# Performance work log

Hardware: AMD Instinct MI355X
Metric: run time of the kernel (lower is better)

## Reference

```python
import jax, jax.numpy as jnp
import numpy as np

N = 16384
C = 4        # in_channels
K = 16       # neighbors
H = 64       # mlp width


def setup_inputs() -> dict:
    key = jax.random.key(0)
    k0, k1, k2, k3, k4 = jax.random.split(key, 5)
    x = jax.random.normal(k0, (N, C), dtype=jnp.float32)
    # nn.Linear(2C, 64) and nn.Linear(64, 64): weight [out, in], bias [out]
    W1 = jax.random.normal(k1, (H, 2 * C), dtype=jnp.float32) * (1.0 / np.sqrt(2 * C))
    b1 = jax.random.normal(k2, (H,), dtype=jnp.float32) * 0.01
    W2 = jax.random.normal(k3, (H, H), dtype=jnp.float32) * (1.0 / np.sqrt(H))
    b2 = jax.random.normal(k4, (H,), dtype=jnp.float32) * 0.01
    return {"x": x, "W1": W1, "b1": b1, "W2": W2, "b2": b2}


def reference(x, W1, b1, W2, b2):
    # x: [N, C] single point cloud (torch code unsqueezes batch dim 0)
    xs = jax.lax.stop_gradient(x)  # knn indices computed under no_grad
    # pairwise = -||xi - xj||^2 = 2*xi.xj - ||xi||^2 - ||xj||^2
    xx = jnp.sum(xs * xs, axis=1)                      # [N]
    pairwise = 2.0 * (xs @ xs.T) - xx[:, None] - xx[None, :]  # [N, N]
    _, idx = jax.lax.top_k(pairwise, K)                # [N, K] (self included, dist 0 is max)
    neigh = x[idx]                                     # [N, K, C] gather
    center = jnp.broadcast_to(x[:, None, :], (x.shape[0], K, C))
    edge = jnp.concatenate([neigh - center, center], axis=-1)  # [N, K, 2C]
    h = jax.nn.relu(jnp.einsum('nkc,hc->nkh', edge, W1) + b1)
    h = jax.nn.relu(jnp.einsum('nkh,gh->nkg', h, W2) + b2)     # [N, K, H]
    out = jnp.mean(h, axis=1)                          # [N, H]
    return out[None]                                   # [1, N, H] matches torch output
```

## Files before the change

### kernel.cpp

```cpp
#include <hip/hip_runtime.h>
#include <math.h>

#define N_PTS 16384
#define K_NBR 16
#define H_DIM 64
#define CAP   78
#define NBLK  (N_PTS / 16)
#define PBLK  (NBLK / 4)

typedef unsigned long long u64;
typedef unsigned short u16;
typedef float v2f   __attribute__((ext_vector_type(2)));
typedef float f32x4 __attribute__((ext_vector_type(4)));
typedef short bf16x8 __attribute__((ext_vector_type(8)));

__device__ __forceinline__ u64 mkkey(unsigned vbits, unsigned idx) {
    unsigned of = vbits ^ (unsigned)(((int)vbits >> 31) | 0x80000000);
    return ((u64)of << 32) | (unsigned)(~idx);
}
__device__ __forceinline__ unsigned keyidx(u64 k) { return ~(unsigned)k; }

__device__ __forceinline__ float readlane_f(float v, int l) {
    return __uint_as_float(__builtin_amdgcn_readlane(__float_as_uint(v), l));
}

__device__ __forceinline__ unsigned ofsbits(float f) {
    unsigned b = __float_as_uint(f);
    return b ^ ((unsigned)((int)b >> 31) | 0x80000000u);
}
__device__ __forceinline__ float inv_ofs(unsigned u) {
    return __uint_as_float(u ^ (~(unsigned)((int)u >> 31) | 0x80000000u));
}

__device__ __forceinline__ u16 f2bf(float f) {
    unsigned u = __float_as_uint(f);
    return (u16)((u + 0x7FFFu + ((u >> 16) & 1u)) >> 16);
}
__device__ __forceinline__ float bf2f(u16 b) {
    return __uint_as_float(((unsigned)b) << 16);
}

__device__ __forceinline__ float wave_sort_f32(float v, int lane) {
#pragma unroll
    for (int k = 2; k <= 64; k <<= 1) {
#pragma unroll
        for (int j = k >> 1; j > 0; j >>= 1) {
            float o = __shfl_xor(v, j, 64);
            bool keep_min = (((lane & k) == 0) == ((lane & j) == 0));
            v = keep_min ? fminf(v, o) : fmaxf(v, o);
        }
    }
    return v;
}
__device__ __forceinline__ u64 wave_sort_u64(u64 v, int lane) {
#pragma unroll
    for (int k = 2; k <= 64; k <<= 1) {
#pragma unroll
        for (int j = k >> 1; j > 0; j >>= 1) {
            u64 o = __shfl_xor((unsigned long long)v, j, 64);
            bool keep_min = (((lane & k) == 0) == ((lane & j) == 0));
            u64 mn = (v < o) ? v : o;
            u64 mx = (v < o) ? o : v;
            v = keep_min ? mn : mx;
        }
    }
    return v;
}

struct CompRes { int nc; float tau; };
__device__ __attribute__((noinline)) CompRes wave_compact(uint2* buf, int cnt,
                                                          int lane) {
    float lm = -INFINITY;
    for (int s = lane; s < cnt; s += 64)
        lm = fmaxf(lm, __uint_as_float(buf[s].x));
    const float tv = readlane_f(wave_sort_f32(lm, lane), 48);
    int nc = 0;
    for (int s0 = 0; s0 < cnt; s0 += 64) {
        const int s = s0 + lane;
        uint2 e = make_uint2(0u, 0u);
        bool keep = false;
        if (s < cnt) { e = buf[s]; keep = (__uint_as_float(e.x) >= tv); }
        const u64 km = __ballot(keep);
        if (keep) {
            int pfx = (int)__popcll(km & ((1ull << lane) - 1));
            buf[nc + pfx] = e;
        }
        nc += (int)__popcll(km);
    }
    CompRes r; r.nc = nc; r.tau = tv;
    return r;
}

__global__ __launch_bounds__(256) void prep_kernel(const float4* __restrict__ x4,
                                                   u16* __restrict__ bf) {
    const int i = blockIdx.x * 256 + threadIdx.x;
    const float4 v = x4[i];
    float xx;
    {
#pragma clang fp contract(off)
        float s0 = v.x * v.x, s1 = v.y * v.y, s2 = v.z * v.z, s3 = v.w * v.w;
        xx = ((s0 + s1) + s2) + s3;
    }
    float c[4] = {v.x, v.y, v.z, v.w};
    u16 H[4], M[4], L[4];
#pragma unroll
    for (int q = 0; q < 4; ++q) {
        float f = c[q];
        u16 h = f2bf(f);            float fh = bf2f(h);
        u16 m = f2bf(f - fh);       float fm = bf2f(m);
        u16 l = f2bf(f - fh - fm);
        H[q] = h; M[q] = m; L[q] = l;
    }
    const float nx = -xx;
    u16 X0 = f2bf(nx);              float x0f = bf2f(X0);
    u16 X1 = f2bf(nx - x0f);        float x1f = bf2f(X1);
    u16 X2 = f2bf(nx - x0f - x1f);
    u16 o[32];
#pragma unroll
    for (int q = 0; q < 4; ++q) {
        o[q]      = H[q];
        o[4 + q]  = M[q];
        o[8 + q]  = H[q];
        o[12 + q] = L[q];
        o[16 + q] = H[q];
        o[20 + q] = M[q];
    }
    o[24] = X0; o[25] = X1; o[26] = X2;
    o[27] = 0; o[28] = 0; o[29] = 0; o[30] = 0; o[31] = 0;
    uint4* dst = (uint4*)(bf + (size_t)i * 32);
#pragma unroll
    for (int q2 = 0; q2 < 4; ++q2) {
        uint4 w;
        w.x = (unsigned)o[q2 * 8 + 0] | ((unsigned)o[q2 * 8 + 1] << 16);
        w.y = (unsigned)o[q2 * 8 + 2] | ((unsigned)o[q2 * 8 + 3] << 16);
        w.z = (unsigned)o[q2 * 8 + 4] | ((unsigned)o[q2 * 8 + 5] << 16);
        w.w = (unsigned)o[q2 * 8 + 6] | ((unsigned)o[q2 * 8 + 7] << 16);
        dst[q2] = w;
    }
}

__global__ __launch_bounds__(256, 4) void knn_kernel(
        const float4* __restrict__ x4,
        const u16* __restrict__ bfrag,
        int* __restrict__ knn) {
    __shared__ __align__(16) uint2 buf[4][16][CAP];
    __shared__ unsigned tau_sh[16];
    const int lane = threadIdx.x & 63;
    const int wave = threadIdx.x >> 6;
    const int q    = lane & 15;
    const int g    = lane >> 4;
    const int rowbase = blockIdx.x * 16;
    const int pblk = wave * PBLK;

    const float4 xi = x4[rowbase + q];
    u16 Ha[4], Ma[4], La[4];
    {
        float yy[4] = {2.f * xi.x, 2.f * xi.y, 2.f * xi.z, 2.f * xi.w};
#pragma unroll
        for (int c = 0; c < 4; ++c) {
            u16 h = f2bf(yy[c]);             float fh = bf2f(h);
            u16 m = f2bf(yy[c] - fh);        float fm = bf2f(m);
            u16 l = f2bf(yy[c] - fh - fm);
            Ha[c] = h; Ma[c] = m; La[c] = l;
        }
    }
    bf16x8 qfrag;
    {
        const u16 ONEB = 0x3F80;
#pragma unroll
        for (int c = 0; c < 4; ++c) {
            u16 lo, hi;
            if (g == 0)      { lo = Ha[c]; hi = Ha[c]; }
            else if (g == 1) { lo = Ma[c]; hi = Ha[c]; }
            else if (g == 2) { lo = La[c]; hi = Ma[c]; }
            else             { lo = (c < 3) ? ONEB : 0; hi = 0; }
            qfrag[c]     = (short)lo;
            qfrag[c + 4] = (short)hi;
        }
    }
    const f32x4 zacc = {0.f, 0.f, 0.f, 0.f};
    const bf16x8* bp = (const bf16x8*)bfrag + (size_t)pblk * 64 + (q * 4 + g);

    f32x4 mx = {-INFINITY, -INFINITY, -INFINITY, -INFINITY};
    {
        bf16x8 A0[4], A1[4];
#pragma unroll
        for (int i = 0; i < 4; ++i) A0[i] = bp[(2 * i) * 64];
#pragma unroll
        for (int i = 0; i < 4; ++i) A1[i] = bp[(8 + 2 * i) * 64];
        const bf16x8* pa = bp + 16 * 64;

#define PROCA(BUF) do {                                                      \
    _Pragma("unroll")                                                        \
    for (int i = 0; i < 4; ++i) {                                            \
        const f32x4 aa = __builtin_amdgcn_mfma_f32_16x16x32_bf16(            \
            BUF[i], qfrag, zacc, 0, 0, 0);                                   \
        mx[0] = fmaxf(mx[0], aa[0]); mx[1] = fmaxf(mx[1], aa[1]);            \
        mx[2] = fmaxf(mx[2], aa[2]); mx[3] = fmaxf(mx[3], aa[3]);            \
    }                                                                        \
} while (0)

        for (int it = 0; it < 15; ++it) {
            PROCA(A0);
#pragma unroll
            for (int i = 0; i < 4; ++i) A0[i] = pa[(2 * i) * 64];
            PROCA(A1);
#pragma unroll
            for (int i = 0; i < 4; ++i) A1[i] = pa[(8 + 2 * i) * 64];
            pa += 16 * 64;
        }
        PROCA(A0);
        PROCA(A1);
#undef PROCA
    }

    {
        float* am = (float*)&buf[0][0][0];
        const int base = wave * 256 + q * 16 + g * 4;
        am[base + 0] = mx[0]; am[base + 1] = mx[1];
        am[base + 2] = mx[2]; am[base + 3] = mx[3];
        __syncthreads();
#pragma unroll
        for (int rr = 0; rr < 4; ++rr) {
            const int r = wave * 4 + rr;
            float v = am[(lane >> 4) * 256 + r * 16 + (lane & 15)];
            v = wave_sort_f32(v, lane);
            if (lane == 48) tau_sh[r] = ofsbits(v);
        }
        __syncthreads();
    }
    float tau = inv_ofs(tau_sh[q]);

    unsigned cq = 0;
    uint2* bq = &buf[wave][q][0];
    const unsigned gid4 = (unsigned)(g * 4);

#define INSERT4(AV, CB) do {                                                 \
    for (;;) {                                                               \
        const bool k0 = (AV)[0] >= tau, k1 = (AV)[1] >= tau;                 \
        const bool k2 = (AV)[2] >= tau, k3 = (AV)[3] >= tau;                 \
        const int cnt = (int)k0 + (int)k1 + (int)k2 + (int)k3;               \
        const int sa = __shfl_xor(cnt, 16, 64);                              \
        const int sb = __shfl_xor(cnt, 32, 64);                              \
        const int sc = __shfl_xor(sa, 32, 64);                               \
        const int tot = cnt + sa + sb + sc;                                  \
        const int pf  = ((g & 1) ? sa : 0) + ((g & 2) ? (sb + sc) : 0);      \
        const u64 ovm = __ballot(cq + (unsigned)tot > CAP);                  \
        if (__builtin_expect(ovm == 0, 1)) {                                 \
            unsigned slot = cq + (unsigned)pf;                               \
            if (k0) bq[slot++] = make_uint2(__float_as_uint((AV)[0]), (CB)); \
            if (k1) bq[slot++] = make_uint2(__float_as_uint((AV)[1]), (CB)+1);\
            if (k2) bq[slot++] = make_uint2(__float_as_uint((AV)[2]), (CB)+2);\
            if (k3) bq[slot++] = make_uint2(__float_as_uint((AV)[3]), (CB)+3);\
            cq += (unsigned)tot;                                             \
            break;                                                           \
        }                                                                    \
        u64 ov = ovm & 0xFFFFull;                                            \
        while (ov) {                                                         \
            const int r = (int)__builtin_ctzll(ov); ov &= ov - 1;            \
            const unsigned cr =                                              \
                (unsigned)__builtin_amdgcn_readlane((int)cq, r);             \
            CompRes res = wave_compact(&buf[wave][r][0], (int)cr, lane);     \
            if (q == r) { cq = (unsigned)res.nc;                             \
                          tau = fmaxf(tau, res.tau); }                       \
        }                                                                    \
    }                                                                        \
} while (0)

#define PROC4(BUF, TB) do {                                                  \
    f32x4 A4_[4];                                                            \
    _Pragma("unroll")                                                        \
    for (int i = 0; i < 4; ++i)                                              \
        A4_[i] = __builtin_amdgcn_mfma_f32_16x16x32_bf16(BUF[i], qfrag,      \
                                                         zacc, 0, 0, 0);     \
    _Pragma("unroll")                                                        \
    for (int i = 0; i < 4; ++i) {                                            \
        const f32x4 av = A4_[i];                                             \
        const float m4 = fmaxf(fmaxf(av[0], av[1]), fmaxf(av[2], av[3]));    \
        if (__ballot(m4 >= tau))                                             \
            INSERT4(av, (unsigned)(((TB) + i) * 16) + gid4);                 \
    }                                                                        \
} while (0)

    {
        bf16x8 B0[4], B1[4];
#pragma unroll
        for (int i = 0; i < 4; ++i) B0[i] = bp[i * 64];
#pragma unroll
        for (int i = 0; i < 4; ++i) B1[i] = bp[(4 + i) * 64];
        const bf16x8* pA = bp + 8 * 64;
        const bf16x8* pB = bp + 12 * 64;

        int t = 0;
        for (; t < PBLK - 8; t += 8) {
            PROC4(B0, pblk + t);
#pragma unroll
            for (int i = 0; i < 4; ++i) B0[i] = pA[i * 64];
            pA += 8 * 64;
            PROC4(B1, pblk + t + 4);
#pragma unroll
            for (int i = 0; i < 4; ++i) B1[i] = pB[i * 64];
            pB += 8 * 64;
        }
        PROC4(B0, pblk + t);
        PROC4(B1, pblk + t + 4);
    }
#undef PROC4
#undef INSERT4

#pragma unroll 1
    for (int r = 0; r < 16; ++r) {
        int c = __builtin_amdgcn_readlane((int)cq, r);
        uint2* br = &buf[wave][r][0];
        if (c > 64) { CompRes res = wave_compact(br, c, lane); c = res.nc; }
        if (c <= 16) {
            if (lane < 16) {
                u64 key = 0;
                if (lane < c) { const uint2 e = br[lane]; key = mkkey(e.x, e.y); }
                *(u64*)&buf[wave][r][lane] = key;
            }
        } else {
            u64 key = 0;
            if (lane < c) { const uint2 e = br[lane]; key = mkkey(e.x, e.y); }
            key = wave_sort_u64(key, lane);
            if (lane >= 48)
                *(u64*)&buf[wave][r][lane - 48] = key;
        }
    }

    __syncthreads();
#pragma unroll
    for (int rr = 0; rr < 4; ++rr) {
        const int r2 = wave * 4 + rr;
        u64 key = *(const u64*)&buf[lane >> 4][r2][lane & 15];
        key = wave_sort_u64(key, lane);
        if (lane >= 48)
            knn[(rowbase + r2) * K_NBR + (lane - 48)] = (int)keyidx(key);
    }
}

__global__ __launch_bounds__(256, 2) void mlp_kernel(
        const float4* __restrict__ x4,
        const int* __restrict__ knn,
        const float4* __restrict__ W2f4,
        const float* __restrict__ W1,
        const float* __restrict__ b1,
        const float* __restrict__ b2,
        float* __restrict__ out) {
    __shared__ __align__(16) float4 w2s[16][64];
    __shared__ __align__(16) float  h1s[4][32][68];
    __shared__ __align__(16) float4 xjs[4][32];
    const int lane = threadIdx.x & 63;
    const int wave = threadIdx.x >> 6;
    const int kq   = lane >> 4;
    const int gp   = lane & 15;
    const int p0   = (blockIdx.x * 4 + wave) * 2;

    for (int q = threadIdx.x; q < 1024; q += 256)
        w2s[q & 15][q >> 4] = W2f4[q];
    __syncthreads();

    float w1r[8];
#pragma unroll
    for (int c = 0; c < 8; ++c) w1r[c] = W1[lane * 8 + c];
    const float b1r = b1[lane];
    float b2r[4];
#pragma unroll
    for (int gq = 0; gq < 4; ++gq) b2r[gq] = b2[gq * 16 + gp];

    if (lane < 32) {
        const int pp = lane >> 4;
        const int nb = knn[(p0 + pp) * K_NBR + (lane & 15)];
        xjs[wave][lane] = x4[nb];
    }

#pragma unroll
    for (int pp = 0; pp < 2; ++pp) {
        const float4 xi = x4[p0 + pp];
        float hb = b1r;
        hb = fmaf(w1r[4] - w1r[0], xi.x, hb);
        hb = fmaf(w1r[5] - w1r[1], xi.y, hb);
        hb = fmaf(w1r[6] - w1r[2], xi.z, hb);
        hb = fmaf(w1r[7] - w1r[3], xi.w, hb);
#pragma unroll
        for (int k = 0; k < K_NBR; ++k) {
            const float4 xj = xjs[wave][pp * 16 + k];
            float h = hb;
            h = fmaf(w1r[0], xj.x, h);
            h = fmaf(w1r[1], xj.y, h);
            h = fmaf(w1r[2], xj.z, h);
            h = fmaf(w1r[3], xj.w, h);
            h1s[wave][pp * 16 + k][lane] = fmaxf(h, 0.0f);
        }
    }

    v2f acc[2][4][4];
#pragma unroll
    for (int pp = 0; pp < 2; ++pp)
#pragma unroll
        for (int kk = 0; kk < 4; ++kk)
#pragma unroll
            for (int gq = 0; gq < 4; ++gq)
                acc[pp][kk][gq] = (v2f){b2r[gq], 0.0f};

#pragma unroll
    for (int h4 = 0; h4 < 16; ++h4) {
        float4 w4[4];
#pragma unroll
        for (int gq = 0; gq < 4; ++gq) w4[gq] = w2s[h4][gq * 16 + gp];
#pragma unroll
        for (int pp = 0; pp < 2; ++pp) {
#pragma unroll
            for (int kk = 0; kk < 4; ++kk) {
                const float4 hv =
                    *(const float4*)&h1s[wave][pp * 16 + kq * 4 + kk][h4 * 4];
#pragma unroll
                for (int gq = 0; gq < 4; ++gq) {
                    acc[pp][kk][gq] = __builtin_elementwise_fma(
                        (v2f){hv.x, hv.y}, (v2f){w4[gq].x, w4[gq].y},
                        acc[pp][kk][gq]);
                    acc[pp][kk][gq] = __builtin_elementwise_fma(
                        (v2f){hv.z, hv.w}, (v2f){w4[gq].z, w4[gq].w},
                        acc[pp][kk][gq]);
                }
            }
        }
    }

#pragma unroll
    for (int pp = 0; pp < 2; ++pp) {
        float s[4];
#pragma unroll
        for (int gq = 0; gq < 4; ++gq) {
            s[gq] = 0.0f;
#pragma unroll
            for (int kk = 0; kk < 4; ++kk) {
                const float v = acc[pp][kk][gq].x + acc[pp][kk][gq].y;
                s[gq] += fmaxf(v, 0.0f);
            }
        }
#pragma unroll
        for (int off = 16; off <= 32; off <<= 1)
#pragma unroll
            for (int gq = 0; gq < 4; ++gq)
                s[gq] += __shfl_xor(s[gq], off, 64);

        out[(p0 + pp) * H_DIM + kq * 16 + gp] = s[kq] * (1.0f / 16.0f);
    }
}

extern "C" void kernel_launch(void* const* d_in, const int* in_sizes, int n_in,
                              void* d_out, int out_size, void* d_ws, size_t ws_size,
                              hipStream_t stream) {
    (void)in_sizes; (void)n_in; (void)out_size; (void)ws_size;
    const float* x  = (const float*)d_in[0];
    const float* W1 = (const float*)d_in[1];
    const float* b1 = (const float*)d_in[2];
    const float* W2 = (const float*)d_in[3];
    const float* b2 = (const float*)d_in[4];
    float* out = (float*)d_out;

    int* knn   = (int*)d_ws;
    u16* bfrag = (u16*)((char*)d_ws + (size_t)N_PTS * K_NBR * sizeof(int));

    const float4* x4 = (const float4*)x;

    prep_kernel<<<N_PTS / 256, 256, 0, stream>>>(x4, bfrag);
    knn_kernel <<<N_PTS / 16,  256, 0, stream>>>(x4, bfrag, knn);
    mlp_kernel <<<N_PTS / 8,   256, 0, stream>>>(
        x4, knn, (const float4*)W2, W1, b1, b2, out);
}
```

Measured before the change: 204.2 us.

## Split kNN candidate scan across two blocks and merge partial top-k in MLP

```diff
diff --git a/kernel.cpp b/kernel.cpp
--- a/kernel.cpp
+++ b/kernel.cpp
@@ -4,9 +4,10 @@
 #define N_PTS 16384
 #define K_NBR 16
 #define H_DIM 64
-#define CAP   78
+#define CAP   48
 #define NBLK  (N_PTS / 16)
-#define PBLK  (NBLK / 4)
+#define HBLK  (NBLK / 2)
+#define PBLK  (HBLK / 4)
 
 typedef unsigned long long u64;
 typedef unsigned short u16;
@@ -59,6 +60,21 @@
         for (int j = k >> 1; j > 0; j >>= 1) {
             u64 o = __shfl_xor((unsigned long long)v, j, 64);
             bool keep_min = (((lane & k) == 0) == ((lane & j) == 0));
+            u64 mn = (v < o) ? v : o;
+            u64 mx = (v < o) ? o : v;
+            v = keep_min ? mn : mx;
+        }
+    }
+    return v;
+}
+__device__ __forceinline__ u64 half32_sort_u64(u64 v, int lane) {
+    const int l = lane & 31;
+#pragma unroll
+    for (int k = 2; k <= 32; k <<= 1) {
+#pragma unroll
+        for (int j = k >> 1; j > 0; j >>= 1) {
+            u64 o = __shfl_xor((unsigned long long)v, j, 64);
+            bool keep_min = (((l & k) == 0) == ((l & j) == 0));
             u64 mn = (v < o) ? v : o;
             u64 mx = (v < o) ? o : v;
             v = keep_min ? mn : mx;
@@ -139,18 +155,21 @@
     }
 }
 
-__global__ __launch_bounds__(256, 4) void knn_kernel(
+__global__ __launch_bounds__(256, 6) void knn_kernel(
         const float4* __restrict__ x4,
         const u16* __restrict__ bfrag,
-        int* __restrict__ knn) {
+        unsigned* __restrict__ vals,
+        u16* __restrict__ idxs) {
     __shared__ __align__(16) uint2 buf[4][16][CAP];
     __shared__ unsigned tau_sh[16];
     const int lane = threadIdx.x & 63;
     const int wave = threadIdx.x >> 6;
     const int q    = lane & 15;
     const int g    = lane >> 4;
-    const int rowbase = blockIdx.x * 16;
-    const int pblk = wave * PBLK;
+    const int qgrp = blockIdx.x >> 1;
+    const int half = blockIdx.x & 1;
+    const int rowbase = qgrp * 16;
+    const int pblk = half * HBLK + wave * PBLK;
 
     const float4 xi = x4[rowbase + q];
     u16 Ha[4], Ma[4], La[4];
@@ -200,7 +219,7 @@
     }                                                                        \
 } while (0)
 
-        for (int it = 0; it < 15; ++it) {
+        for (int it = 0; it < 7; ++it) {
             PROCA(A0);
 #pragma unroll
             for (int i = 0; i < 4; ++i) A0[i] = pa[(2 * i) * 64];
@@ -312,7 +331,6 @@
     for (int r = 0; r < 16; ++r) {
         int c = __builtin_amdgcn_readlane((int)cq, r);
         uint2* br = &buf[wave][r][0];
-        if (c > 64) { CompRes res = wave_compact(br, c, lane); c = res.nc; }
         if (c <= 16) {
             if (lane < 16) {
                 u64 key = 0;
@@ -334,14 +352,18 @@
         const int r2 = wave * 4 + rr;
         u64 key = *(const u64*)&buf[lane >> 4][r2][lane & 15];
         key = wave_sort_u64(key, lane);
-        if (lane >= 48)
-            knn[(rowbase + r2) * K_NBR + (lane - 48)] = (int)keyidx(key);
+        if (lane >= 48) {
+            const int o = (rowbase + r2) * 32 + half * 16 + (lane - 48);
+            vals[o] = (unsigned)(key >> 32);
+            idxs[o] = (u16)keyidx(key);
+        }
     }
 }
 
 __global__ __launch_bounds__(256, 2) void mlp_kernel(
         const float4* __restrict__ x4,
-        const int* __restrict__ knn,
+        const unsigned* __restrict__ vals,
+        const u16* __restrict__ idxs,
         const float4* __restrict__ W2f4,
         const float* __restrict__ W1,
         const float* __restrict__ b1,
@@ -368,10 +390,16 @@
 #pragma unroll
     for (int gq = 0; gq < 4; ++gq) b2r[gq] = b2[gq * 16 + gp];
 
-    if (lane < 32) {
-        const int pp = lane >> 4;
-        const int nb = knn[(p0 + pp) * K_NBR + (lane & 15)];
-        xjs[wave][lane] = x4[nb];
+    {
+        const int pp = lane >> 5;
+        const int j  = lane & 31;
+        const int o  = (p0 + pp) * 32 + j;
+        u64 key = ((u64)vals[o] << 32) | (unsigned)(~(unsigned)idxs[o]);
+        key = half32_sort_u64(key, lane);
+        if ((lane & 31) >= 16) {
+            const int nb = (int)((~(unsigned)key) & 0xFFFFu);
+            xjs[wave][pp * 16 + ((lane & 31) - 16)] = x4[nb];
+        }
     }
 
 #pragma unroll
@@ -460,13 +488,14 @@
     const float* b2 = (const float*)d_in[4];
     float* out = (float*)d_out;
 
-    int* knn   = (int*)d_ws;
-    u16* bfrag = (u16*)((char*)d_ws + (size_t)N_PTS * K_NBR * sizeof(int));
+    u16*      bfrag = (u16*)d_ws;
+    unsigned* vals  = (unsigned*)((char*)d_ws + (1u << 20));
+    u16*      idxs  = (u16*)((char*)d_ws + (3u << 20));
 
     const float4* x4 = (const float4*)x;
 
     prep_kernel<<<N_PTS / 256, 256, 0, stream>>>(x4, bfrag);
-    knn_kernel <<<N_PTS / 16,  256, 0, stream>>>(x4, bfrag, knn);
+    knn_kernel <<<N_PTS / 16 * 2, 256, 0, stream>>>(x4, bfrag, vals, idxs);
     mlp_kernel <<<N_PTS / 8,   256, 0, stream>>>(
-        x4, knn, (const float4*)W2, W1, b1, b2, out);
-}
+        x4, vals, idxs, (const float4*)W2, W1, b1, b2, out);
+}
```

Result: slower. 220.0 us (+7.8%).
